# Kernel optimization log

Hardware: AMD Instinct MI355X
Metric: run time of the kernel (lower is better)

The kernel has to match this reference:

```python
import jax, jax.numpy as jnp
import numpy as np

OBS, ACT, EMB, HID, NQ = 512, 32, 512, 512, 32
B = 32768


def setup_inputs() -> dict:
    key = jax.random.key(0)
    ks = jax.random.split(key, 12)
    s_in = 1.0 / np.sqrt(OBS + ACT)
    s_emb = 1.0 / np.sqrt(EMB)
    s_hid = 1.0 / np.sqrt(HID)
    return {
        "observation": jax.random.normal(ks[0], (B, OBS), jnp.float32),
        "prev_action": jax.random.normal(ks[1], (B, ACT), jnp.float32),
        "hidden_state": jax.random.normal(ks[2], (HID,), jnp.float32),
        "cell_state": jax.random.normal(ks[3], (HID,), jnp.float32),
        "W1": jax.random.uniform(ks[4], (EMB, OBS + ACT), jnp.float32, -s_in, s_in),
        "b1": jax.random.uniform(ks[5], (EMB,), jnp.float32, -s_in, s_in),
        "W_ih": jax.random.uniform(ks[6], (4 * HID, EMB), jnp.float32, -s_hid, s_hid),
        "b_ih": jax.random.uniform(ks[7], (4 * HID,), jnp.float32, -s_hid, s_hid),
        "W_hh": jax.random.uniform(ks[8], (4 * HID, HID), jnp.float32, -s_hid, s_hid),
        "b_hh": jax.random.uniform(ks[9], (4 * HID,), jnp.float32, -s_hid, s_hid),
        "W2": jax.random.uniform(ks[10], (NQ, HID), jnp.float32, -s_hid, s_hid),
        "b2": jax.random.uniform(ks[11], (NQ,), jnp.float32, -s_hid, s_hid),
    }


def reference(observation, prev_action, hidden_state, cell_state,
              W1, b1, W_ih, b_ih, W_hh, b_hh, W2, b2):
    # MLP1: Linear + ReLU over concat(obs, prev_action)  -> [B, EMB]
    x = jnp.concatenate([observation, prev_action], axis=-1)
    x = jax.nn.relu(x @ W1.T + b1)

    # Original torch code loops LSTMCell over batch, but reuses the SAME
    # (hidden_state, cell_state) every iteration -> fully batchable.
    # gates: [B, 4H]; h contribution is identical for all rows (broadcast).
    gates = x @ W_ih.T + b_ih + (hidden_state @ W_hh.T + b_hh)
    i, f, g, o = jnp.split(gates, 4, axis=-1)  # torch LSTMCell gate order
    i = jax.nn.sigmoid(i)
    f = jax.nn.sigmoid(f)
    g = jnp.tanh(g)
    o = jax.nn.sigmoid(o)
    c_new = f * cell_state + i * g          # [B, HID]
    h_new = o * jnp.tanh(c_new)             # [B, HID]

    q_values = h_new @ W2.T + b2             # [B, NQ]
    # torch returns last loop iteration's (h, c)
    return q_values, h_new[-1], c_new[-1]
```

## Files before the change

kernel.cpp:

```cpp
#include <hip/hip_runtime.h>
#include <stdint.h>

#define DEVINL __device__ __forceinline__

typedef __attribute__((ext_vector_type(8))) __bf16 bf16x8;
typedef __attribute__((ext_vector_type(4))) float f32x4;
typedef __attribute__((ext_vector_type(2))) long longx2;

DEVINL unsigned short f2bf(float f) {
  union { float f; unsigned int u; } v; v.f = f;
  unsigned int u = v.u;
  return (unsigned short)((u + 0x7fffu + ((u >> 16) & 1u)) >> 16);
}

DEVINL unsigned char f2fp8(float f) {
  return (unsigned char)(__builtin_amdgcn_cvt_pk_fp8_f32(f, f, 0, false) & 0xff);
}

DEVINL float sigm(float x) { return __builtin_amdgcn_rcpf(1.f + __expf(-x)); }
DEVINL float tanh_(float x) {
  return 1.f - 2.f * __builtin_amdgcn_rcpf(1.f + __expf(2.f * x));
}

DEVINL int pcol(int gn) {
  return (gn & ~63) | ((((gn & 31) >> 3)) << 4) | (((gn >> 5) & 1) << 3) | (gn & 7);
}

#define GLD_LDS16(gptr, lptr)                                                  \
  __builtin_amdgcn_global_load_lds(                                            \
      (__attribute__((address_space(1))) void*)(gptr),                         \
      (__attribute__((address_space(3))) void*)(lptr), 16, 0, 0)

#define TOPBAR_4 asm volatile("s_waitcnt vmcnt(4) lgkmcnt(0)\n\ts_barrier" ::: "memory")
#define TOPBAR_1 asm volatile("s_waitcnt vmcnt(1) lgkmcnt(0)\n\ts_barrier" ::: "memory")
#define TOPBAR_0 asm volatile("s_waitcnt vmcnt(0) lgkmcnt(0)\n\ts_barrier" ::: "memory")
#define BOTBAR   asm volatile("s_waitcnt lgkmcnt(0)\n\ts_barrier" ::: "memory")

DEVINL int swz_col(int c) { return ((c & 3) ^ ((c >> 3) & 3)) * 8; }
DEVINL int swz16(int c) { return ((c & 3) ^ ((c >> 3) & 3)) * 16; }

__global__ void prep_all(const float* __restrict__ obs, const float* __restrict__ act,
                         const float* __restrict__ W1, const float* __restrict__ Wih,
                         const float* __restrict__ W2, const float* __restrict__ Whh,
                         const float* __restrict__ hid, const float* __restrict__ bhh,
                         const float* __restrict__ bih,
                         unsigned short* __restrict__ A0, unsigned short* __restrict__ W1b,
                         unsigned char* __restrict__ Wih8, unsigned short* __restrict__ W2b,
                         float* __restrict__ hvec) {
  const int bid = blockIdx.x, tid = threadIdx.x;
  if (bid < 2176) {
    const int total = 32768 * 68;
    for (int c = bid * 256 + tid; c < total; c += 2176 * 256) {
      const int b = c / 68, c8 = c % 68;
      const float* src = (c8 < 64) ? (obs + (size_t)b * 512 + c8 * 8)
                                   : (act + (size_t)b * 32 + (c8 - 64) * 8);
      float4 f0 = *(const float4*)src;
      float4 f1 = *(const float4*)(src + 4);
      unsigned short u[8] = {f2bf(f0.x), f2bf(f0.y), f2bf(f0.z), f2bf(f0.w),
                             f2bf(f1.x), f2bf(f1.y), f2bf(f1.z), f2bf(f1.w)};
      *(uint4*)(A0 + (size_t)b * 544 + c8 * 8) = *(uint4*)u;
    }
  } else if (bid < 2176 + 1312) {
    const int i = (bid - 2176) * 256 + tid;
    if (i < 69632) {
      float4 f = *(const float4*)(W1 + (size_t)i * 4);
      unsigned short u[4] = {f2bf(f.x), f2bf(f.y), f2bf(f.z), f2bf(f.w)};
      *(uint2*)(W1b + (size_t)i * 4) = *(uint2*)u;
    } else if (i < 69632 + 262144) {
      const int off = i - 69632;
      const int row = off >> 7, col0 = (off & 127) * 4;
      float4 f = *(const float4*)(Wih + (size_t)off * 4);
      int pk = __builtin_amdgcn_cvt_pk_fp8_f32(f.x * 16.f, f.y * 16.f, 0, false);
      pk = __builtin_amdgcn_cvt_pk_fp8_f32(f.z * 16.f, f.w * 16.f, pk, true);
      *(unsigned int*)(Wih8 + (size_t)row * 512 + pcol(col0)) = (unsigned int)pk;
    } else {
      const int off = i - 331776;
      float4 f = *(const float4*)(W2 + (size_t)off * 4);
      unsigned short u[4] = {f2bf(f.x), f2bf(f.y), f2bf(f.z), f2bf(f.w)};
      *(uint2*)(W2b + (size_t)off * 4) = *(uint2*)u;
    }
  } else {
    const int j = (bid - 3488) * 4 + (tid >> 6);
    const int lane = tid & 63;
    const float* w = Whh + (size_t)j * 512;
    float s = 0.f;
    for (int k = lane; k < 512; k += 64) s += w[k] * hid[k];
    for (int off = 32; off; off >>= 1) s += __shfl_down(s, off, 64);
    if (lane == 0) hvec[j] = s + bhh[j] + bih[j];
  }
}

__global__ __launch_bounds__(256, 2) void gemm1_relu(
    const unsigned short* __restrict__ A0,
    const unsigned short* __restrict__ W1b,
    const float* __restrict__ b1,
    unsigned char* __restrict__ X8) {
  constexpr int KT = 17, LD = 544;
  __shared__ __align__(16) unsigned short As[2][128 * 32];
  __shared__ __align__(16) unsigned short Bs[2][128 * 32];
  const int tid = threadIdx.x, wave = tid >> 6, lane = tid & 63;
  const int id = blockIdx.x, xcd = id & 7, slot = id >> 3;
  const int m0 = (xcd * 32 + (slot >> 2)) * 128;
  const int n0 = (slot & 3) * 128;
  const int wr = (wave >> 1) * 64, wc = (wave & 1) * 64;
  f32x4 acc[4][4] = {};

  const int c0 = tid, c1 = tid + 256;
  const unsigned short* pA0 = A0 + (size_t)(m0 + (c0 >> 2)) * LD + swz_col(c0);
  const unsigned short* pA1 = A0 + (size_t)(m0 + (c1 >> 2)) * LD + swz_col(c1);
  const unsigned short* pB0 = W1b + (size_t)(n0 + (c0 >> 2)) * LD + swz_col(c0);
  const unsigned short* pB1 = W1b + (size_t)(n0 + (c1 >> 2)) * LD + swz_col(c1);
  const int fr = lane & 15, q = lane >> 4;
  const int koff = (q ^ ((fr >> 1) & 3)) * 8;

#define STAGE1(buf)                                                            \
  do {                                                                         \
    GLD_LDS16(pA0, &As[(buf)][wave * 512]);                                    \
    GLD_LDS16(pA1, &As[(buf)][2048 + wave * 512]);                             \
    GLD_LDS16(pB0, &Bs[(buf)][wave * 512]);                                    \
    GLD_LDS16(pB1, &Bs[(buf)][2048 + wave * 512]);                             \
    pA0 += 32; pA1 += 32; pB0 += 32; pB1 += 32;                                \
  } while (0)

  STAGE1(0);
  for (int kt = 0; kt < KT; ++kt) {
    if (kt + 1 < KT) { STAGE1((kt + 1) & 1); TOPBAR_4; } else { TOPBAR_0; }
    const unsigned short* as = As[kt & 1];
    const unsigned short* bs = Bs[kt & 1];
    bf16x8 a[4], b[4];
#pragma unroll
    for (int i = 0; i < 4; ++i) a[i] = *(const bf16x8*)&as[(wr + i * 16 + fr) * 32 + koff];
#pragma unroll
    for (int j = 0; j < 4; ++j) b[j] = *(const bf16x8*)&bs[(wc + j * 16 + fr) * 32 + koff];
#pragma unroll
    for (int i = 0; i < 4; ++i)
#pragma unroll
      for (int j = 0; j < 4; ++j)
        acc[i][j] = __builtin_amdgcn_mfma_f32_16x16x32_bf16(a[i], b[j], acc[i][j], 0, 0, 0);
    BOTBAR;
  }
#undef STAGE1
  const int rbase = q * 4, cn = fr;
#pragma unroll
  for (int i = 0; i < 4; ++i)
#pragma unroll
    for (int j = 0; j < 4; ++j) {
      const int gn = n0 + wc + j * 16 + cn;
      const int pc = pcol(gn);
      const float bias = b1[gn];
#pragma unroll
      for (int r = 0; r < 4; ++r) {
        const int gm = m0 + wr + i * 16 + rbase + r;
        float v = acc[i][j][r] + bias;
        v = v > 0.f ? v : 0.f;
        X8[(size_t)gm * 512 + pc] = f2fp8(v * 8.f);
      }
    }
}

__global__ __launch_bounds__(256, 4) void gemm2_lstm(
    const unsigned char* __restrict__ X8,
    const unsigned char* __restrict__ Wih8,
    const float* __restrict__ hvec,
    const float* __restrict__ cell,
    unsigned short* __restrict__ H,
    float* __restrict__ hlast,
    float* __restrict__ clast) {
  constexpr int KT = 8;
  __shared__ __align__(16) unsigned char As[2][128 * 64];
  __shared__ __align__(16) unsigned char Bs[2][4 * 32 * 64];
  const int tid = threadIdx.x, wave = tid >> 6, lane = tid & 63;
  const int id = blockIdx.x, xcd = id & 7, slot = id >> 3;
  const int m0 = (xcd * 32 + (slot >> 4)) * 128;
  const int n0 = (slot & 15) * 32;
  const int wr = (wave >> 1) * 64, wc = (wave & 1) * 16;
  f32x4 acc[4][4] = {};

  const int c0 = tid, c1 = tid + 256;
  const unsigned char* pA0 = X8 + (size_t)(m0 + (c0 >> 2)) * 512 + swz16(c0);
  const unsigned char* pA1 = X8 + (size_t)(m0 + (c1 >> 2)) * 512 + swz16(c1);
  const unsigned char* pB0 =
      Wih8 + (size_t)((c0 >> 7) * 512 + n0 + ((c0 >> 2) & 31)) * 512 + swz16(c0);
  const unsigned char* pB1 =
      Wih8 + (size_t)((c1 >> 7) * 512 + n0 + ((c1 >> 2) & 31)) * 512 + swz16(c1);
  const int fr = lane & 15, q = lane >> 4;
  const int koff = (q ^ ((fr >> 1) & 3)) * 16;

#define STAGE2(buf)                                                            \
  do {                                                                         \
    GLD_LDS16(pA0, &As[(buf)][wave * 1024]);                                   \
    GLD_LDS16(pA1, &As[(buf)][4096 + wave * 1024]);                            \
    GLD_LDS16(pB0, &Bs[(buf)][wave * 1024]);                                   \
    GLD_LDS16(pB1, &Bs[(buf)][4096 + wave * 1024]);                            \
    pA0 += 64; pA1 += 64; pB0 += 64; pB1 += 64;                                \
  } while (0)

  STAGE2(0);
  for (int kt = 0; kt < KT; ++kt) {
    if (kt + 1 < KT) { STAGE2((kt + 1) & 1); TOPBAR_4; } else { TOPBAR_0; }
    const unsigned char* as = As[kt & 1];
    const unsigned char* bs = Bs[kt & 1];
    longx2 a[4], b[4];
#pragma unroll
    for (int i = 0; i < 4; ++i)
      a[i] = *(const longx2*)&as[(wr + i * 16 + fr) * 64 + koff];
#pragma unroll
    for (int qd = 0; qd < 4; ++qd)
      b[qd] = *(const longx2*)&bs[qd * 2048 + (wc + fr) * 64 + koff];
#pragma unroll
    for (int i = 0; i < 4; ++i)
#pragma unroll
      for (int qd = 0; qd < 4; ++qd) {
        acc[i][qd] =
            __builtin_amdgcn_mfma_f32_16x16x32_fp8_fp8(a[i].x, b[qd].x, acc[i][qd], 0, 0, 0);
        acc[i][qd] =
            __builtin_amdgcn_mfma_f32_16x16x32_fp8_fp8(a[i].y, b[qd].y, acc[i][qd], 0, 0, 0);
      }
    BOTBAR;
  }
#undef STAGE2
  const int rbase = q * 4, cn = fr;
  const int gn = n0 + wc + cn;
  const float hv_i = hvec[gn];
  const float hv_f = hvec[gn + 512];
  const float hv_g = hvec[gn + 1024];
  const float hv_o = hvec[gn + 1536];
  const float cprev = cell[gn];
  constexpr float S = 1.f / 128.f;
#pragma unroll
  for (int i = 0; i < 4; ++i)
#pragma unroll
    for (int r = 0; r < 4; ++r) {
      const int gm = m0 + wr + i * 16 + rbase + r;
      float si = sigm(acc[i][0][r] * S + hv_i);
      float sf = sigm(acc[i][1][r] * S + hv_f);
      float tg = tanh_(acc[i][2][r] * S + hv_g);
      float so = sigm(acc[i][3][r] * S + hv_o);
      float cnew = sf * cprev + si * tg;
      float hnew = so * tanh_(cnew);
      H[(size_t)gm * 512 + gn] = f2bf(hnew);
      if (gm == 32767) { hlast[gn] = hnew; clast[gn] = cnew; }
    }
}

__global__ __launch_bounds__(256, 2) void gemm3(
    const unsigned short* __restrict__ H,
    const unsigned short* __restrict__ W2b,
    const float* __restrict__ b2,
    float* __restrict__ Q) {
  constexpr int KT = 16, LDW = 520;
  __shared__ __align__(16) unsigned short As[2][64 * 32];
  __shared__ __align__(16) unsigned short Ws[32 * LDW];
  const int tid = threadIdx.x, wave = tid >> 6, lane = tid & 63;
  const int id = blockIdx.x;
  const int m0 = ((id & 7) * 64 + (id >> 3)) * 64;
  for (int c = tid; c < 2048; c += 256) {
    const int row = c >> 6, col8 = c & 63;
    *(uint4*)&Ws[row * LDW + col8 * 8] = *(const uint4*)(W2b + row * 512 + col8 * 8);
  }
  f32x4 acc[2] = {};
  const int c0 = tid;
  const unsigned short* pA0 = H + (size_t)(m0 + (c0 >> 2)) * 512 + swz_col(c0);
  const int fr = lane & 15, q = lane >> 4;
  const int koff = (q ^ ((fr >> 1) & 3)) * 8;

#define STAGE3(buf)                                                            \
  do {                                                                         \
    GLD_LDS16(pA0, &As[(buf)][wave * 512]);                                    \
    pA0 += 32;                                                                 \
  } while (0)

  STAGE3(0);
  for (int kt = 0; kt < KT; ++kt) {
    if (kt + 1 < KT) { STAGE3((kt + 1) & 1); TOPBAR_1; } else { TOPBAR_0; }
    const unsigned short* as = As[kt & 1];
    const int k0 = kt * 32;
    bf16x8 a  = *(const bf16x8*)&as[(wave * 16 + fr) * 32 + koff];
    bf16x8 b0 = *(const bf16x8*)&Ws[fr * LDW + k0 + q * 8];
    bf16x8 b1 = *(const bf16x8*)&Ws[(16 + fr) * LDW + k0 + q * 8];
    acc[0] = __builtin_amdgcn_mfma_f32_16x16x32_bf16(a, b0, acc[0], 0, 0, 0);
    acc[1] = __builtin_amdgcn_mfma_f32_16x16x32_bf16(a, b1, acc[1], 0, 0, 0);
    BOTBAR;
  }
#undef STAGE3
  const int rbase = q * 4;
#pragma unroll
  for (int j = 0; j < 2; ++j) {
    const int gn = j * 16 + fr;
    const float bias = b2[gn];
#pragma unroll
    for (int r = 0; r < 4; ++r) {
      const int gm = m0 + wave * 16 + rbase + r;
      Q[(size_t)gm * 32 + gn] = acc[j][r] + bias;
    }
  }
}

extern "C" void kernel_launch(void* const* d_in, const int* in_sizes, int n_in,
                              void* d_out, int out_size, void* d_ws, size_t ws_size,
                              hipStream_t stream) {
  const float* obs  = (const float*)d_in[0];
  const float* act  = (const float*)d_in[1];
  const float* hid  = (const float*)d_in[2];
  const float* cell = (const float*)d_in[3];
  const float* W1   = (const float*)d_in[4];
  const float* b1   = (const float*)d_in[5];
  const float* Wih  = (const float*)d_in[6];
  const float* bih  = (const float*)d_in[7];
  const float* Whh  = (const float*)d_in[8];
  const float* bhh  = (const float*)d_in[9];
  const float* W2   = (const float*)d_in[10];
  const float* b2   = (const float*)d_in[11];
  float* out = (float*)d_out;

  char* ws = (char*)d_ws;
  unsigned short* A0   = (unsigned short*)(ws);
  unsigned short* H    = (unsigned short*)(ws);
  unsigned char*  X8   = (unsigned char*)(ws + 35651584);
  unsigned short* W1b  = (unsigned short*)(ws + 52428800);
  unsigned char*  Wih8 = (unsigned char*)(ws + 52985856);
  unsigned short* W2b  = (unsigned short*)(ws + 54034432);
  float*          hvec = (float*)(ws + 54067200);

  prep_all<<<4000, 256, 0, stream>>>(obs, act, W1, Wih, W2, Whh, hid, bhh, bih,
                                     A0, W1b, Wih8, W2b, hvec);
  gemm1_relu<<<1024, 256, 0, stream>>>(A0, W1b, b1, X8);
  gemm2_lstm<<<4096, 256, 0, stream>>>(X8, Wih8, hvec, cell, H,
                                       out + 32768 * 32,
                                       out + 32768 * 32 + 512);
  gemm3<<<512, 256, 0, stream>>>(H, W2b, b2, out);
}
```

Baseline: 213.4 us.

## Use 32x32x64 scaled FP8 MFMA in LSTM gate GEMM and drop column permutation

Replaces the pairs of 16x16x32 FP8 MFMAs in the LSTM gate GEMM with the gfx950 32x32x64 f8f6f4 scaled MFMA, using unit scales (0x7f) so results match. Each wave now owns a 32-row by 32-column tile for all four gates, and the LDS fragment loads and epilogue row/column mapping are rewritten to fit. The pcol column permutation applied when writing Wih8 and X8 is removed, because the new fragment layout reads contiguous k-chunks. Occupancy is lowered to 3 blocks per CU, since the larger accumulators use more registers.

Result: no change. 216.5 us (+1.5%).

```diff
diff --git a/kernel.cpp b/kernel.cpp
--- a/kernel.cpp
+++ b/kernel.cpp
@@ -5,7 +5,9 @@
 
 typedef __attribute__((ext_vector_type(8))) __bf16 bf16x8;
 typedef __attribute__((ext_vector_type(4))) float f32x4;
-typedef __attribute__((ext_vector_type(2))) long longx2;
+typedef __attribute__((ext_vector_type(16))) float f32x16;
+typedef __attribute__((ext_vector_type(4))) int i32x4;
+typedef __attribute__((ext_vector_type(8))) int i32x8;
 
 DEVINL unsigned short f2bf(float f) {
   union { float f; unsigned int u; } v; v.f = f;
@@ -20,10 +22,6 @@
 DEVINL float sigm(float x) { return __builtin_amdgcn_rcpf(1.f + __expf(-x)); }
 DEVINL float tanh_(float x) {
   return 1.f - 2.f * __builtin_amdgcn_rcpf(1.f + __expf(2.f * x));
-}
-
-DEVINL int pcol(int gn) {
-  return (gn & ~63) | ((((gn & 31) >> 3)) << 4) | (((gn >> 5) & 1) << 3) | (gn & 7);
 }
 
 #define GLD_LDS16(gptr, lptr)                                                  \
@@ -72,7 +70,7 @@
       float4 f = *(const float4*)(Wih + (size_t)off * 4);
       int pk = __builtin_amdgcn_cvt_pk_fp8_f32(f.x * 16.f, f.y * 16.f, 0, false);
       pk = __builtin_amdgcn_cvt_pk_fp8_f32(f.z * 16.f, f.w * 16.f, pk, true);
-      *(unsigned int*)(Wih8 + (size_t)row * 512 + pcol(col0)) = (unsigned int)pk;
+      *(unsigned int*)(Wih8 + (size_t)row * 512 + col0) = (unsigned int)pk;
     } else {
       const int off = i - 331776;
       float4 f = *(const float4*)(W2 + (size_t)off * 4);
@@ -146,19 +144,18 @@
 #pragma unroll
     for (int j = 0; j < 4; ++j) {
       const int gn = n0 + wc + j * 16 + cn;
-      const int pc = pcol(gn);
       const float bias = b1[gn];
 #pragma unroll
       for (int r = 0; r < 4; ++r) {
         const int gm = m0 + wr + i * 16 + rbase + r;
         float v = acc[i][j][r] + bias;
         v = v > 0.f ? v : 0.f;
-        X8[(size_t)gm * 512 + pc] = f2fp8(v * 8.f);
+        X8[(size_t)gm * 512 + gn] = f2fp8(v * 8.f);
       }
     }
 }
 
-__global__ __launch_bounds__(256, 4) void gemm2_lstm(
+__global__ __launch_bounds__(256, 3) void gemm2_lstm(
     const unsigned char* __restrict__ X8,
     const unsigned char* __restrict__ Wih8,
     const float* __restrict__ hvec,
@@ -173,8 +170,7 @@
   const int id = blockIdx.x, xcd = id & 7, slot = id >> 3;
   const int m0 = (xcd * 32 + (slot >> 4)) * 128;
   const int n0 = (slot & 15) * 32;
-  const int wr = (wave >> 1) * 64, wc = (wave & 1) * 16;
-  f32x4 acc[4][4] = {};
+  f32x16 acc[4] = {};
 
   const int c0 = tid, c1 = tid + 256;
   const unsigned char* pA0 = X8 + (size_t)(m0 + (c0 >> 2)) * 512 + swz16(c0);
@@ -183,8 +179,12 @@
       Wih8 + (size_t)((c0 >> 7) * 512 + n0 + ((c0 >> 2) & 31)) * 512 + swz16(c0);
   const unsigned char* pB1 =
       Wih8 + (size_t)((c1 >> 7) * 512 + n0 + ((c1 >> 2) & 31)) * 512 + swz16(c1);
-  const int fr = lane & 15, q = lane >> 4;
-  const int koff = (q ^ ((fr >> 1) & 3)) * 16;
+
+  const int r31 = lane & 31, g2 = lane >> 5;
+  const int sw = (r31 >> 1) & 3;
+  const int plo = ((2 * g2) ^ sw) * 16, phi = ((2 * g2 + 1) ^ sw) * 16;
+  const int arow = (wave * 32 + r31) * 64;
+  const int brow = r31 * 64;
 
 #define STAGE2(buf)                                                            \
   do {                                                                         \
@@ -200,27 +200,28 @@
     if (kt + 1 < KT) { STAGE2((kt + 1) & 1); TOPBAR_4; } else { TOPBAR_0; }
     const unsigned char* as = As[kt & 1];
     const unsigned char* bs = Bs[kt & 1];
-    longx2 a[4], b[4];
-#pragma unroll
-    for (int i = 0; i < 4; ++i)
-      a[i] = *(const longx2*)&as[(wr + i * 16 + fr) * 64 + koff];
+    i32x4 alo = *(const i32x4*)&as[arow + plo];
+    i32x4 ahi = *(const i32x4*)&as[arow + phi];
+    i32x8 a = __builtin_shufflevector(alo, ahi, 0, 1, 2, 3, 4, 5, 6, 7);
+    i32x8 b[4];
+#pragma unroll
+    for (int qd = 0; qd < 4; ++qd) {
+      i32x4 blo = *(const i32x4*)&bs[qd * 2048 + brow + plo];
+      i32x4 bhi = *(const i32x4*)&bs[qd * 2048 + brow + phi];
+      b[qd] = __builtin_shufflevector(blo, bhi, 0, 1, 2, 3, 4, 5, 6, 7);
+    }
 #pragma unroll
     for (int qd = 0; qd < 4; ++qd)
-      b[qd] = *(const longx2*)&bs[qd * 2048 + (wc + fr) * 64 + koff];
-#pragma unroll
-    for (int i = 0; i < 4; ++i)
-#pragma unroll
-      for (int qd = 0; qd < 4; ++qd) {
-        acc[i][qd] =
-            __builtin_amdgcn_mfma_f32_16x16x32_fp8_fp8(a[i].x, b[qd].x, acc[i][qd], 0, 0, 0);
-        acc[i][qd] =
-            __builtin_amdgcn_mfma_f32_16x16x32_fp8_fp8(a[i].y, b[qd].y, acc[i][qd], 0, 0, 0);
-      }
+      acc[qd] = __builtin_amdgcn_mfma_scale_f32_32x32x64_f8f6f4(
+          a, b[qd], acc[qd],
+          0, 0,
+          0, 0x7f7f7f7f,
+          0, 0x7f7f7f7f);
     BOTBAR;
   }
 #undef STAGE2
-  const int rbase = q * 4, cn = fr;
-  const int gn = n0 + wc + cn;
+
+  const int gn = n0 + r31;
   const float hv_i = hvec[gn];
   const float hv_f = hvec[gn + 512];
   const float hv_g = hvec[gn + 1024];
@@ -228,14 +229,15 @@
   const float cprev = cell[gn];
   constexpr float S = 1.f / 128.f;
 #pragma unroll
-  for (int i = 0; i < 4; ++i)
-#pragma unroll
-    for (int r = 0; r < 4; ++r) {
-      const int gm = m0 + wr + i * 16 + rbase + r;
-      float si = sigm(acc[i][0][r] * S + hv_i);
-      float sf = sigm(acc[i][1][r] * S + hv_f);
-      float tg = tanh_(acc[i][2][r] * S + hv_g);
-      float so = sigm(acc[i][3][r] * S + hv_o);
+  for (int rg = 0; rg < 4; ++rg)
+#pragma unroll
+    for (int rr = 0; rr < 4; ++rr) {
+      const int reg = rg * 4 + rr;
+      const int gm = m0 + wave * 32 + rr + rg * 8 + g2 * 4;
+      float si = sigm(acc[0][reg] * S + hv_i);
+      float sf = sigm(acc[1][reg] * S + hv_f);
+      float tg = tanh_(acc[2][reg] * S + hv_g);
+      float so = sigm(acc[3][reg] * S + hv_o);
       float cnew = sf * cprev + si * tg;
       float hnew = so * tanh_(cnew);
       H[(size_t)gm * 512 + gn] = f2bf(hnew);
```
